# Kernel optimization log

Hardware: AMD Instinct MI355X
Metric: run time of the kernel (lower is better)

## Reference

```python
import jax, jax.numpy as jnp
import numpy as np

H = 768      # hidden_size
NH = 12      # num_heads
HD = H // NH # head_size
MLP = 3072
B, N = 16, 577


def setup_inputs() -> dict:
    key = jax.random.key(0)
    ks = jax.random.split(key, 16)
    s = 0.02
    return {
        "x": jax.random.normal(ks[0], (B, N, H), jnp.float32),
        "Wq": jax.random.normal(ks[1], (H, H), jnp.float32) * s,
        "bq": jnp.zeros((H,), jnp.float32),
        "Wk": jax.random.normal(ks[2], (H, H), jnp.float32) * s,
        "bk": jnp.zeros((H,), jnp.float32),
        "Wv": jax.random.normal(ks[3], (H, H), jnp.float32) * s,
        "bv": jnp.zeros((H,), jnp.float32),
        "Wo": jax.random.normal(ks[4], (H, H), jnp.float32) * s,
        "bo": jnp.zeros((H,), jnp.float32),
        "W1": jax.random.normal(ks[5], (H, MLP), jnp.float32) * s,
        "b1": jnp.zeros((MLP,), jnp.float32),
        "W2": jax.random.normal(ks[6], (MLP, H), jnp.float32) * s,
        "b2": jnp.zeros((H,), jnp.float32),
        "ln1_g": jnp.ones((H,), jnp.float32),
        "ln1_b": jnp.zeros((H,), jnp.float32),
        "ln2_g": jnp.ones((H,), jnp.float32),
        "ln2_b": jnp.zeros((H,), jnp.float32),
    }


def _layernorm(x, g, b, eps=1e-6):
    mu = jnp.mean(x, axis=-1, keepdims=True)
    var = jnp.mean(jnp.square(x - mu), axis=-1, keepdims=True)
    return (x - mu) * jax.lax.rsqrt(var + eps) * g + b


def reference(x, Wq, bq, Wk, bk, Wv, bv, Wo, bo, W1, b1, W2, b2,
              ln1_g, ln1_b, ln2_g, ln2_b):
    h = x
    y = _layernorm(x, ln1_g, ln1_b)
    # projections [B,N,H] -> [B,NH,N,HD]
    def heads(t):
        return t.reshape(B, N, NH, HD).transpose(0, 2, 1, 3)
    q = heads(y @ Wq + bq)
    _k = heads(y @ Wk + bk)  # computed but UNUSED (bug in original: Q@V^T)
    v = heads(y @ Wv + bv)
    # faithful to source: scores = Q @ V^T (not K)
    scores = jnp.einsum('bhqd,bhkd->bhqk', q, v) / jnp.sqrt(jnp.float32(HD))
    probs = jax.nn.softmax(scores, axis=-1)
    o = jnp.einsum('bhqk,bhkd->bhqd', probs, v)
    o = o.transpose(0, 2, 1, 3).reshape(B, N, H)
    attn_out = o @ Wo + bo
    x1 = attn_out + h
    h2 = x1
    y2 = _layernorm(x1, ln2_g, ln2_b)
    m = jax.nn.gelu(y2 @ W1 + b1, approximate=False)
    m = m @ W2 + b2
    return m + h2
```

## Files before the change

### kernel.cpp

```cpp
#include <hip/hip_runtime.h>


#define GLOBAL_AS __attribute__((address_space(1)))
#define LDS_AS __attribute__((address_space(3)))

typedef __bf16 bf16x8 __attribute__((ext_vector_type(8)));
typedef float f32x4 __attribute__((ext_vector_type(4)));
typedef unsigned short u16x8 __attribute__((ext_vector_type(8)));

static __device__ __forceinline__ f32x4 mfma16(bf16x8 a, bf16x8 b, f32x4 c) {
  return __builtin_amdgcn_mfma_f32_16x16x32_bf16(a, b, c, 0, 0, 0);
}

static __device__ __forceinline__ unsigned short f2bf(float f) {
  union { float f; unsigned u; } v; v.f = f;
  unsigned r = v.u + 0x7fffu + ((v.u >> 16) & 1u);
  return (unsigned short)(r >> 16);
}

static __device__ __forceinline__ void async16(const void* g, void* l) {
  __builtin_amdgcn_global_load_lds((const GLOBAL_AS void*)g, (LDS_AS void*)l, 16, 0, 0);
}

static __device__ __forceinline__ float gelu_exact(float x) {
  return 0.5f * x * (1.0f + erff(x * 0.70710678118654752f));
}

static __device__ __forceinline__ void tc_body(const float* __restrict__ W,
                                               unsigned short* __restrict__ Wt,
                                               int K, int ldw, int nb, int kb,
                                               int t) {
  __shared__ float tile[32][33];
  const int tr = t >> 5, tc = t & 31;
#pragma unroll
  for (int p = 0; p < 4; ++p)
    tile[p * 8 + tr][tc] = W[(size_t)(kb + p * 8 + tr) * ldw + nb + tc];
  __syncthreads();
#pragma unroll
  for (int p = 0; p < 4; ++p)
    Wt[(size_t)(nb + p * 8 + tr) * K + kb + tc] = f2bf(tile[tc][p * 8 + tr]);
}

__global__ __launch_bounds__(256)
void transpose_all(const float* __restrict__ Wq, const float* __restrict__ Wv,
                   const float* __restrict__ Wo, const float* __restrict__ W1,
                   const float* __restrict__ W2, unsigned short* __restrict__ R3) {
  const size_t S = 589824;
  int id = blockIdx.x;
  const int t = threadIdx.x;
  if (id < 1728) {
    const float* W = id < 576 ? Wq : (id < 1152 ? Wv : Wo);
    unsigned short* dst = R3 + (size_t)(id / 576) * S;
    id %= 576;
    tc_body(W, dst, 768, 768, (id % 24) * 32, (id / 24) * 32, t);
  } else {
    id -= 1728;
    const int seg = id / 1152;
    id %= 1152;
    const int s = seg >> 1;
    if ((seg & 1) == 0) {
      unsigned short* dst = R3 + 3 * S + (size_t)s * 4 * S;
      tc_body(W1 + s * 1536, dst, 768, 3072, (id % 48) * 32, (id / 48) * 32, t);
    } else {
      unsigned short* dst = R3 + 5 * S + (size_t)s * 4 * S;
      tc_body(W2 + (size_t)s * 1536 * 768, dst, 1536, 768, (id % 24) * 32,
              (id / 24) * 32, t);
    }
  }
}

__global__ __launch_bounds__(256)
void ln_f32(const float* __restrict__ x, const float* __restrict__ g,
            const float* __restrict__ be, unsigned short* __restrict__ y) {
  const int w = threadIdx.x >> 6, lane = threadIdx.x & 63;
  const size_t row = (size_t)blockIdx.x * 4 + w;
  const float* xr = x + row * 768;
  float vv[12];
#pragma unroll
  for (int j = 0; j < 3; ++j) {
    float4 v = *(const float4*)(xr + j * 256 + lane * 4);
    vv[j * 4 + 0] = v.x; vv[j * 4 + 1] = v.y;
    vv[j * 4 + 2] = v.z; vv[j * 4 + 3] = v.w;
  }
  float s = 0.f;
#pragma unroll
  for (int j = 0; j < 12; ++j) s += vv[j];
#pragma unroll
  for (int o = 32; o > 0; o >>= 1) s += __shfl_xor(s, o);
  const float mu = s * (1.0f / 768.0f);
  float q = 0.f;
#pragma unroll
  for (int j = 0; j < 12; ++j) { float d = vv[j] - mu; q += d * d; }
#pragma unroll
  for (int o = 32; o > 0; o >>= 1) q += __shfl_xor(q, o);
  const float rstd = rsqrtf(q * (1.0f / 768.0f) + 1e-6f);
  unsigned short* yr = y + row * 768;
#pragma unroll
  for (int j = 0; j < 3; ++j) {
    float4 gv = *(const float4*)(g + j * 256 + lane * 4);
    float4 bv = *(const float4*)(be + j * 256 + lane * 4);
    ushort4 o4;
    o4.x = f2bf((vv[j * 4 + 0] - mu) * rstd * gv.x + bv.x);
    o4.y = f2bf((vv[j * 4 + 1] - mu) * rstd * gv.y + bv.y);
    o4.z = f2bf((vv[j * 4 + 2] - mu) * rstd * gv.z + bv.z);
    o4.w = f2bf((vv[j * 4 + 3] - mu) * rstd * gv.w + bv.w);
    *(ushort4*)(yr + j * 256 + lane * 4) = o4;
  }
}

template <int ACT, int RES, int OUTF32, int NB, int SPLIT>
__global__ __launch_bounds__(512, 1)
void gemm_bt(const unsigned short* __restrict__ A,
             const unsigned short* __restrict__ B,
             const float* __restrict__ bias,
             const float* __restrict__ bias2,
             const float* __restrict__ resid,
             void* __restrict__ out1, void* __restrict__ out2,
             int M, int N, int K) {
  __shared__ __align__(16) unsigned short As[2][128 * 32];
  __shared__ __align__(16) unsigned short Bs[2][256 * 32];
  const int t = threadIdx.x;
  const int nwg = gridDim.x;
  const int q8 = nwg >> 3, r8 = nwg & 7;
  const int xcd = blockIdx.x & 7, jj = blockIdx.x >> 3;
  const int wgid = (xcd < r8 ? xcd * (q8 + 1) : r8 * (q8 + 1) + (xcd - r8) * q8) + jj;
  const int gn = N >> 8;
  const int m0 = (wgid / gn) * 128;
  const int n0 = (wgid % gn) * 256;
  const int w = t >> 6, lane = t & 63;
  const int lr = lane & 15, lg = lane >> 4;
  const int wrr = (w >> 2) * 64;
  const int wcc = (w & 3) * 64;
  f32x4 acc[4][4] = {};

  auto stage = [&](int buf, int k0) {
    {
      int i = t;
      int row = i >> 2, c = (i & 3) << 3;
      int ar = m0 + row; ar = ar < M ? ar : M - 1;
      async16(A + (size_t)ar * K + k0 + c, &As[buf][i * 8]);
    }
#pragma unroll
    for (int p = 0; p < 2; ++p) {
      int i = p * 512 + t;
      int row = i >> 2, c = (i & 3) << 3;
      async16(B + (size_t)(n0 + row) * K + k0 + c, &Bs[buf][i * 8]);
    }
  };

  stage(0, 0);
  int cur = 0;
  const int nt = K >> 5;
  for (int tt = 0; tt < nt; ++tt) {
    if (tt + 1 < nt) {
      stage(cur ^ 1, (tt + 1) << 5);
      asm volatile("s_waitcnt vmcnt(3)" ::: "memory");
    } else {
      asm volatile("s_waitcnt vmcnt(0)" ::: "memory");
    }
    __builtin_amdgcn_s_barrier();
    bf16x8 af[4], bfr[4];
#pragma unroll
    for (int mi = 0; mi < 4; ++mi)
      af[mi] = *(const bf16x8*)(&As[cur][(wrr + mi * 16 + lr) * 32 + lg * 8]);
#pragma unroll
    for (int ni = 0; ni < 4; ++ni)
      bfr[ni] = *(const bf16x8*)(&Bs[cur][(wcc + ni * 16 + lr) * 32 + lg * 8]);
    asm volatile("s_waitcnt lgkmcnt(0)" ::: "memory");
    __builtin_amdgcn_sched_barrier(0);
    __builtin_amdgcn_s_barrier();
#pragma unroll
    for (int mi = 0; mi < 4; ++mi)
#pragma unroll
      for (int ni = 0; ni < 4; ++ni)
        acc[mi][ni] = mfma16(af[mi], bfr[ni], acc[mi][ni]);
    cur ^= 1;
  }
  const int orow = m0 + wrr + lg * 4;
  const int ocol = n0 + wcc + lr;
#pragma unroll
  for (int mi = 0; mi < 4; ++mi) {
#pragma unroll
    for (int ni = 0; ni < 4; ++ni) {
      const int col = ocol + ni * 16;
      float bs;
      if (SPLIT)
        bs = (col < 768) ? bias[col] : bias2[col - 768];
      else
        bs = NB ? 0.f : bias[col];
      f32x4 a = acc[mi][ni];
#pragma unroll
      for (int r = 0; r < 4; ++r) {
        const int row = orow + mi * 16 + r;
        if (row < M) {
          float v = a[r] + bs;
          if (ACT == 1) v = gelu_exact(v);
          if (RES == 1) v += resid[(size_t)row * N + col];
          if (SPLIT) {
            if (col < 768)
              ((unsigned short*)out1)[(size_t)row * 768 + col] = f2bf(v);
            else
              ((unsigned short*)out2)[(size_t)row * 768 + col - 768] = f2bf(v);
          } else if (OUTF32) {
            ((float*)out1)[(size_t)row * N + col] = v;
          } else {
            ((unsigned short*)out1)[(size_t)row * N + col] = f2bf(v);
          }
        }
      }
    }
  }
}

__global__ __launch_bounds__(256, 2)
void attn_fused(const unsigned short* __restrict__ Q,
                const unsigned short* __restrict__ V,
                unsigned short* __restrict__ O) {
  __shared__ __align__(16) unsigned short Vn[64 * 72];
  __shared__ __align__(16) unsigned short Vt[64 * 72];
  __shared__ __align__(16) unsigned short Pl[4][32 * 72];
  const int qt = blockIdx.x, h = blockIdx.y, b = blockIdx.z;
  const int t = threadIdx.x, w = t >> 6, lane = t & 63;
  const int lr = lane & 15, lg = lane >> 4;
  const int q0 = qt * 128 + w * 32;
  bf16x8 aq[2][2];
#pragma unroll
  for (int mi = 0; mi < 2; ++mi) {
    int qrow = q0 + mi * 16 + lr; qrow = qrow < 577 ? qrow : 576;
    const unsigned short* qp = Q + ((size_t)(b * 577 + qrow)) * 768 + h * 64;
    aq[mi][0] = *(const bf16x8*)(qp + lg * 8);
    aq[mi][1] = *(const bf16x8*)(qp + 32 + lg * 8);
  }
  bf16x8 ones;
#pragma unroll
  for (int j = 0; j < 8; ++j) ones[j] = (__bf16)1.0f;
  f32x4 oacc[2][4] = {};
  f32x4 lac[2] = {};
  const unsigned short* vp = V + (size_t)b * 577 * 768 + h * 64;

  for (int kt = 0; kt < 10; ++kt) {
    const int k0 = kt * 64;
#pragma unroll
    for (int p = 0; p < 2; ++p) {
      int i = p * 256 + t;
      int kr = i >> 3, c = (i & 7) << 3;
      int gk = k0 + kr; gk = gk < 577 ? gk : 576;
      bf16x8 vv = *(const bf16x8*)(vp + (size_t)gk * 768 + c);
      *(bf16x8*)(Vn + kr * 72 + c) = vv;
    }
    __syncthreads();
#pragma unroll
    for (int p = 0; p < 2; ++p) {
      int i = p * 256 + t;
      int d = i & 63, kb = (i >> 6) * 8;
      u16x8 tv;
#pragma unroll
      for (int j = 0; j < 8; ++j) tv[j] = Vn[(kb + j) * 72 + d];
      *(u16x8*)(Vt + d * 72 + kb) = tv;
    }
    f32x4 s[2][4];
#pragma unroll
    for (int mi = 0; mi < 2; ++mi)
#pragma unroll
      for (int ni = 0; ni < 4; ++ni) {
        f32x4 a = {};
        a = mfma16(aq[mi][0], *(const bf16x8*)(Vn + (ni * 16 + lr) * 72 + lg * 8), a);
        a = mfma16(aq[mi][1], *(const bf16x8*)(Vn + (ni * 16 + lr) * 72 + 32 + lg * 8), a);
        s[mi][ni] = a * 0.125f;
      }
    if (kt == 9) {
#pragma unroll
      for (int ni = 0; ni < 4; ++ni) {
        int kc = k0 + ni * 16 + lr;
        if (kc >= 577) {
#pragma unroll
          for (int mi = 0; mi < 2; ++mi) {
            s[mi][ni][0] = -1e30f; s[mi][ni][1] = -1e30f;
            s[mi][ni][2] = -1e30f; s[mi][ni][3] = -1e30f;
          }
        }
      }
    }
#pragma unroll
    for (int mi = 0; mi < 2; ++mi)
#pragma unroll
      for (int ni = 0; ni < 4; ++ni)
#pragma unroll
        for (int r = 0; r < 4; ++r)
          Pl[w][(mi * 16 + lg * 4 + r) * 72 + ni * 16 + lr] =
              f2bf(__expf(s[mi][ni][r]));
    __syncthreads();
#pragma unroll
    for (int mi = 0; mi < 2; ++mi) {
      const bf16x8 pa0 = *(const bf16x8*)(&Pl[w][(mi * 16 + lr) * 72 + lg * 8]);
      const bf16x8 pa1 = *(const bf16x8*)(&Pl[w][(mi * 16 + lr) * 72 + 32 + lg * 8]);
#pragma unroll
      for (int di = 0; di < 4; ++di) {
        oacc[mi][di] = mfma16(pa0, *(const bf16x8*)(Vt + (di * 16 + lr) * 72 + lg * 8), oacc[mi][di]);
        oacc[mi][di] = mfma16(pa1, *(const bf16x8*)(Vt + (di * 16 + lr) * 72 + 32 + lg * 8), oacc[mi][di]);
      }
      lac[mi] = mfma16(pa0, ones, lac[mi]);
      lac[mi] = mfma16(pa1, ones, lac[mi]);
    }
  }
#pragma unroll
  for (int mi = 0; mi < 2; ++mi)
#pragma unroll
    for (int r = 0; r < 4; ++r) {
      const int qg = q0 + mi * 16 + lg * 4 + r;
      if (qg < 577) {
        const float inv = 1.0f / lac[mi][r];
        unsigned short* op = O + ((size_t)(b * 577 + qg)) * 768 + h * 64 + lr;
#pragma unroll
        for (int di = 0; di < 4; ++di) op[di * 16] = f2bf(oacc[mi][di][r] * inv);
      }
    }
}

extern "C" void kernel_launch(void* const* d_in, const int* in_sizes, int n_in,
                              void* d_out, int out_size, void* d_ws, size_t ws_size,
                              hipStream_t stream) {
  (void)in_sizes; (void)n_in; (void)out_size; (void)ws_size;
  const float* x   = (const float*)d_in[0];
  const float* Wq  = (const float*)d_in[1];
  const float* bq  = (const float*)d_in[2];
  const float* Wv  = (const float*)d_in[5];
  const float* bv  = (const float*)d_in[6];
  const float* Wo  = (const float*)d_in[7];
  const float* bo  = (const float*)d_in[8];
  const float* W1  = (const float*)d_in[9];
  const float* b1  = (const float*)d_in[10];
  const float* W2  = (const float*)d_in[11];
  const float* b2  = (const float*)d_in[12];
  const float* g1  = (const float*)d_in[13];
  const float* be1 = (const float*)d_in[14];
  const float* g2  = (const float*)d_in[15];
  const float* be2 = (const float*)d_in[16];
  float* out = (float*)d_out;

  const size_t BF = (size_t)9232 * 768 * 2;
  const size_t S = 589824;
  char* ws = (char*)d_ws;
  unsigned short* R0 = (unsigned short*)(ws);
  unsigned short* R1 = (unsigned short*)(ws + BF);
  unsigned short* R2 = (unsigned short*)(ws + 2 * BF);
  unsigned short* R3 = (unsigned short*)(ws + 3 * BF);
  unsigned short* WqT = R3;
  unsigned short* WoT = R3 + 2 * S;
  unsigned short* W1T0 = R3 + 3 * S;
  unsigned short* W2T0 = R3 + 5 * S;
  unsigned short* W1T1 = R3 + 7 * S;
  unsigned short* W2T1 = R3 + 9 * S;
  unsigned short* mb = R1;

  dim3 blk(256);
  dim3 blk512(512);

  transpose_all<<<dim3(6336), blk, 0, stream>>>(Wq, Wv, Wo, W1, W2, R3);

  ln_f32<<<dim3(2308), blk, 0, stream>>>(x, g1, be1, R0);

  gemm_bt<0, 0, 0, 0, 1><<<dim3(438), blk512, 0, stream>>>(
      R0, WqT, bq, bv, nullptr, R1, R2, 9232, 1536, 768);

  attn_fused<<<dim3(5, 12, 16), blk, 0, stream>>>(R1, R2, R0);

  gemm_bt<0, 1, 1, 0, 0><<<dim3(219), blk512, 0, stream>>>(
      R0, WoT, bo, nullptr, x, out, nullptr, 9232, 768, 768);

  ln_f32<<<dim3(2308), blk, 0, stream>>>(out, g2, be2, R0);

  gemm_bt<1, 0, 0, 0, 0><<<dim3(438), blk512, 0, stream>>>(
      R0, W1T0, b1, nullptr, nullptr, mb, nullptr, 9232, 1536, 768);
  gemm_bt<0, 1, 1, 0, 0><<<dim3(219), blk512, 0, stream>>>(
      mb, W2T0, b2, nullptr, out, out, nullptr, 9232, 768, 1536);
  gemm_bt<1, 0, 0, 0, 0><<<dim3(438), blk512, 0, stream>>>(
      R0, W1T1, b1 + 1536, nullptr, nullptr, mb, nullptr, 9232, 1536, 768);
  gemm_bt<0, 1, 1, 1, 0><<<dim3(219), blk512, 0, stream>>>(
      mb, W2T1, nullptr, nullptr, out, out, nullptr, 9232, 768, 1536);
}
```

Measured before the change: 341.2 us.

## Triple-buffer GEMM with 64-wide K tiles and XOR-swizzled LDS layout

Reworks the bf16 GEMM main loop. The K tile grows from 32 to 64, and LDS becomes a three-stage ring, so loads run two tiles ahead with one barrier per tile instead of two. The LDS columns are XOR-swizzled on the global-side address to reduce bank conflicts on the MFMA fragment reads, and source pointers are precomputed outside the loop. The cost is about 147 KB of LDS per workgroup, and the loop is manually unrolled by 3, which assumes K/64 is a multiple of 3.

Result: slower. 350.4 us (+2.7%).

```diff
diff --git a/kernel.cpp b/kernel.cpp
--- a/kernel.cpp
+++ b/kernel.cpp
@@ -117,8 +117,8 @@
              const float* __restrict__ resid,
              void* __restrict__ out1, void* __restrict__ out2,
              int M, int N, int K) {
-  __shared__ __align__(16) unsigned short As[2][128 * 32];
-  __shared__ __align__(16) unsigned short Bs[2][256 * 32];
+  __shared__ __align__(16) unsigned short As[3][128 * 64];
+  __shared__ __align__(16) unsigned short Bs[3][256 * 64];
   const int t = threadIdx.x;
   const int nwg = gridDim.x;
   const int q8 = nwg >> 3, r8 = nwg & 7;
@@ -133,49 +133,63 @@
   const int wcc = (w & 3) * 64;
   f32x4 acc[4][4] = {};
 
+  int aOff[2], bOff[4];
+  const unsigned short* aSrc[2];
+  const unsigned short* bSrc[4];
+#pragma unroll
+  for (int p = 0; p < 2; ++p) {
+    int i = p * 512 + t, row = i >> 3, c = ((i ^ row) & 7) << 3;
+    int ar = m0 + row; ar = ar < M ? ar : M - 1;
+    aOff[p] = i * 8;
+    aSrc[p] = A + (size_t)ar * K + c;
+  }
+#pragma unroll
+  for (int p = 0; p < 4; ++p) {
+    int i = p * 512 + t, row = i >> 3, c = ((i ^ row) & 7) << 3;
+    bOff[p] = i * 8;
+    bSrc[p] = B + (size_t)(n0 + row) * K + c;
+  }
   auto stage = [&](int buf, int k0) {
-    {
-      int i = t;
-      int row = i >> 2, c = (i & 3) << 3;
-      int ar = m0 + row; ar = ar < M ? ar : M - 1;
-      async16(A + (size_t)ar * K + k0 + c, &As[buf][i * 8]);
-    }
-#pragma unroll
-    for (int p = 0; p < 2; ++p) {
-      int i = p * 512 + t;
-      int row = i >> 2, c = (i & 3) << 3;
-      async16(B + (size_t)(n0 + row) * K + k0 + c, &Bs[buf][i * 8]);
-    }
+#pragma unroll
+    for (int p = 0; p < 2; ++p) async16(aSrc[p] + k0, &As[buf][aOff[p]]);
+#pragma unroll
+    for (int p = 0; p < 4; ++p) async16(bSrc[p] + k0, &Bs[buf][bOff[p]]);
   };
 
+  const int nt = K >> 6;
   stage(0, 0);
-  int cur = 0;
-  const int nt = K >> 5;
-  for (int tt = 0; tt < nt; ++tt) {
-    if (tt + 1 < nt) {
-      stage(cur ^ 1, (tt + 1) << 5);
-      asm volatile("s_waitcnt vmcnt(3)" ::: "memory");
-    } else {
-      asm volatile("s_waitcnt vmcnt(0)" ::: "memory");
-    }
-    __builtin_amdgcn_s_barrier();
-    bf16x8 af[4], bfr[4];
-#pragma unroll
-    for (int mi = 0; mi < 4; ++mi)
-      af[mi] = *(const bf16x8*)(&As[cur][(wrr + mi * 16 + lr) * 32 + lg * 8]);
-#pragma unroll
-    for (int ni = 0; ni < 4; ++ni)
-      bfr[ni] = *(const bf16x8*)(&Bs[cur][(wcc + ni * 16 + lr) * 32 + lg * 8]);
-    asm volatile("s_waitcnt lgkmcnt(0)" ::: "memory");
-    __builtin_amdgcn_sched_barrier(0);
-    __builtin_amdgcn_s_barrier();
-#pragma unroll
-    for (int mi = 0; mi < 4; ++mi)
-#pragma unroll
-      for (int ni = 0; ni < 4; ++ni)
-        acc[mi][ni] = mfma16(af[mi], bfr[ni], acc[mi][ni]);
-    cur ^= 1;
-  }
+  stage(1, 64);
+
+#define TILE_BODY(BUF, TT)                                                    \
+  {                                                                           \
+    if ((TT) + 1 < nt)                                                        \
+      asm volatile("s_waitcnt vmcnt(6)" ::: "memory");    \
+    else                                                                      \
+      asm volatile("s_waitcnt vmcnt(0)" ::: "memory");                        \
+    __builtin_amdgcn_s_barrier();  \
+    if ((TT) + 2 < nt) stage(((BUF) + 2) % 3, ((TT) + 2) << 6);               \
+    bf16x8 af[2][4], bfr[2][4];                                               \
+    _Pragma("unroll") for (int kk = 0; kk < 2; ++kk) {                        \
+      _Pragma("unroll") for (int mi = 0; mi < 4; ++mi)                        \
+        af[kk][mi] = *(const bf16x8*)(&As[BUF][(wrr + mi * 16 + lr) * 64 +    \
+                                      (((kk << 2) | lg) ^ (lr & 7)) * 8]);    \
+      _Pragma("unroll") for (int ni = 0; ni < 4; ++ni)                        \
+        bfr[kk][ni] = *(const bf16x8*)(&Bs[BUF][(wcc + ni * 16 + lr) * 64 +   \
+                                      (((kk << 2) | lg) ^ (lr & 7)) * 8]);    \
+    }                                                                         \
+    _Pragma("unroll") for (int kk = 0; kk < 2; ++kk)                          \
+      _Pragma("unroll") for (int mi = 0; mi < 4; ++mi)                        \
+        _Pragma("unroll") for (int ni = 0; ni < 4; ++ni)                      \
+          acc[mi][ni] = mfma16(af[kk][mi], bfr[kk][ni], acc[mi][ni]);         \
+  }
+
+  for (int tt = 0; tt < nt; tt += 3) {
+    TILE_BODY(0, tt);
+    TILE_BODY(1, tt + 1);
+    TILE_BODY(2, tt + 2);
+  }
+#undef TILE_BODY
+
   const int orow = m0 + wrr + lg * 4;
   const int ocol = n0 + wcc + lr;
 #pragma unroll
```
